# Kernel tuning notes

Measured on AMD Instinct MI355X. Metric: run time of the kernel, lower is better.

## Reference

```python
import jax, jax.numpy as jnp
import numpy as np

NUM_GROUPS = 32
EPS = 1e-8


def stratified_norm(x, s):
    # Per-group mean and (unbiased, ddof=1, matching torch.std) standard deviation,
    # computed with segment sums, then gathered back per sample.
    ones = jnp.ones((x.shape[0],), dtype=x.dtype)
    cnt = jax.ops.segment_sum(ones, s, num_segments=NUM_GROUPS)  # [G]
    mu = jax.ops.segment_sum(x, s, num_segments=NUM_GROUPS) / jnp.maximum(cnt, 1.0)[:, None]  # [G, D]
    diff = x - mu[s]  # [N, D]
    var = jax.ops.segment_sum(diff * diff, s, num_segments=NUM_GROUPS) / jnp.maximum(cnt - 1.0, 1.0)[:, None]
    std = jnp.sqrt(var)  # [G, D]
    return diff / (std[s] + EPS)


def leaky_relu(x):
    return jnp.where(x >= 0, x, 0.01 * x)


def setup_inputs() -> dict:
    key = jax.random.key(0)
    ks = jax.random.split(key, 10)
    N = 524288
    x = jax.random.normal(ks[0], (N, 248), dtype=jnp.float32)
    i = jax.random.randint(ks[1], (N,), 0, NUM_GROUPS, dtype=jnp.int32)
    def lin(kw, kb, fan_in, fan_out):
        bound = 1.0 / np.sqrt(fan_in)
        W = jax.random.uniform(kw, (fan_out, fan_in), jnp.float32, -bound, bound)
        b = jax.random.uniform(kb, (fan_out,), jnp.float32, -bound, bound)
        return W, b
    W1, b1 = lin(ks[2], ks[3], 248, 64)
    W2, b2 = lin(ks[4], ks[5], 64, 64)
    W3, b3 = lin(ks[6], ks[7], 64, 64)
    W4, b4 = lin(ks[8], ks[9], 64, 3)
    return {"x": x, "i": i, "W1": W1, "b1": b1, "W2": W2, "b2": b2,
            "W3": W3, "b3": b3, "W4": W4, "b4": b4}


def reference(x, i, W1, b1, W2, b2, W3, b3, W4, b4):
    # Dropout layers act as identity at inference.
    z = stratified_norm(leaky_relu(x @ W1.T + b1), i)
    z = stratified_norm(leaky_relu(z @ W2.T + b2), i)
    z = stratified_norm(leaky_relu(z @ W3.T + b3), i)
    z = z @ W4.T + b4
    return z
```

## Files before the change

### kernel.cpp

```cpp
#include <hip/hip_runtime.h>


#define GRP_N 32
#define EPSV 1e-8f
constexpr int DIN = 248;
constexpr int KP  = 256;
constexpr int H   = 64;
constexpr int ASTR = 40;

typedef __attribute__((ext_vector_type(8))) short short8;
typedef __attribute__((ext_vector_type(4))) float f32x4;

__device__ __forceinline__ void mfma_bf16(f32x4& d, short8 a, short8 b) {
    asm volatile("v_mfma_f32_16x16x32_bf16 %0, %1, %2, %0"
                 : "+v"(d) : "v"(a), "v"(b));
}

__device__ __forceinline__ unsigned short f2bf(float f) {
    unsigned u = __float_as_uint(f);
    return (unsigned short)((u + 0x7FFFu + ((u >> 16) & 1u)) >> 16);
}
__device__ __forceinline__ float bf2f(unsigned short h) {
    return __uint_as_float((unsigned)h << 16);
}

__global__ void prep_weights(const float* __restrict__ W1, const float* __restrict__ W2,
                             const float* __restrict__ W3, const float* __restrict__ W4,
                             unsigned short* __restrict__ W1bh, unsigned short* __restrict__ W1bl,
                             float* __restrict__ W2T, float* __restrict__ W3T,
                             float* __restrict__ W4T) {
    int idx = blockIdx.x * blockDim.x + threadIdx.x;
    int stride = gridDim.x * blockDim.x;
    for (int t = idx; t < H * KP; t += stride) {
        int c = t >> 8, k = t & 255;
        float v = (k < DIN) ? W1[c * DIN + k] : 0.f;
        unsigned short hi = f2bf(v);
        W1bh[t] = hi;
        W1bl[t] = f2bf(v - bf2f(hi));
    }
    for (int t = idx; t < H * H; t += stride) {
        int k = t / H, c = t % H;
        W2T[t] = W2[c * H + k];
        W3T[t] = W3[c * H + k];
    }
    for (int t = idx; t < H * 3; t += stride) {
        int k = t / 3, o = t % 3;
        W4T[t] = W4[o * H + k];
    }
}

__global__ __launch_bounds__(256)
void gemm1_mfma(const float* __restrict__ x,
                const unsigned short* __restrict__ W1bh, const unsigned short* __restrict__ W1bl,
                const float* __restrict__ b1, const int* __restrict__ grp,
                float* __restrict__ Y, float* __restrict__ sum_, float* __restrict__ sq_,
                int* __restrict__ cnt, int ntiles) {
    __shared__ unsigned short Ah[128 * ASTR];
    __shared__ unsigned short Al[128 * ASTR];
    __shared__ unsigned short Bh[64 * ASTR];
    __shared__ unsigned short Bl[64 * ASTR];
    __shared__ float sS[GRP_N * H];
    __shared__ float sQ[GRP_N * H];
    __shared__ int gl[128];
    __shared__ int cS[GRP_N];
    const int tid = threadIdx.x;
    const int lane = tid & 63, w = tid >> 6;
    const int l15 = lane & 15, lq = lane >> 4;
    for (int t = tid; t < GRP_N * H; t += 256) { sS[t] = 0.f; sQ[t] = 0.f; }
    if (tid < GRP_N) cS[tid] = 0;

    const int arow = tid >> 1;
    const int akb  = (tid & 1) * 16;
    const int bcol = tid >> 2;
    const int bkb  = (tid & 3) * 8;

    float bias4[4];
#pragma unroll
    for (int cf = 0; cf < 4; ++cf) bias4[cf] = b1[cf * 16 + l15];

    for (int tile = blockIdx.x; tile < ntiles; tile += gridDim.x) {
        const int row0 = tile << 7;
        int g = 0;
        if (tid < 128) g = grp[row0 + tid];
        const float* xrow = x + (size_t)(row0 + arow) * DIN;

        float xv[16];
#pragma unroll
        for (int q = 0; q < 4; ++q) {
            const int kg = akb + q * 4;
            float4 t4 = (kg < DIN) ? *(const float4*)(xrow + kg) : make_float4(0.f, 0.f, 0.f, 0.f);
            xv[q * 4 + 0] = t4.x; xv[q * 4 + 1] = t4.y;
            xv[q * 4 + 2] = t4.z; xv[q * 4 + 3] = t4.w;
        }
        float4 wh = *(const float4*)(W1bh + bcol * KP + bkb);
        float4 wl = *(const float4*)(W1bl + bcol * KP + bkb);

        __syncthreads();
        if (tid < 128) { gl[tid] = g; atomicAdd(&cS[g], 1); }

        f32x4 acc[2][4];
#pragma unroll
        for (int rf = 0; rf < 2; ++rf)
#pragma unroll
            for (int cf = 0; cf < 4; ++cf) acc[rf][cf] = (f32x4){0.f, 0.f, 0.f, 0.f};

#pragma unroll 1
        for (int ch = 0; ch < 8; ++ch) {
            if (ch) __syncthreads();
#pragma unroll
            for (int q = 0; q < 4; ++q) {
                unsigned short h[4], l[4];
#pragma unroll
                for (int j = 0; j < 4; ++j) {
                    float v = xv[q * 4 + j];
                    h[j] = f2bf(v);
                    l[j] = f2bf(v - bf2f(h[j]));
                }
                const int aoff = arow * ASTR + akb + q * 4;
                *(ushort4*)&Ah[aoff] = make_ushort4(h[0], h[1], h[2], h[3]);
                *(ushort4*)&Al[aoff] = make_ushort4(l[0], l[1], l[2], l[3]);
            }
            const int boff = bcol * ASTR + bkb;
            *(float4*)&Bh[boff] = wh;
            *(float4*)&Bl[boff] = wl;
            __syncthreads();
            if (ch < 7) {
                const int kc = (ch + 1) * 32;
#pragma unroll
                for (int q = 0; q < 4; ++q) {
                    const int kg = kc + akb + q * 4;
                    float4 t4 = (kg < DIN) ? *(const float4*)(xrow + kg)
                                           : make_float4(0.f, 0.f, 0.f, 0.f);
                    xv[q * 4 + 0] = t4.x; xv[q * 4 + 1] = t4.y;
                    xv[q * 4 + 2] = t4.z; xv[q * 4 + 3] = t4.w;
                }
                wh = *(const float4*)(W1bh + bcol * KP + kc + bkb);
                wl = *(const float4*)(W1bl + bcol * KP + kc + bkb);
            }
            short8 afh[2], afl[2], bfh[4], bfl[4];
#pragma unroll
            for (int rf = 0; rf < 2; ++rf) {
                const int ar = w * 32 + rf * 16 + l15;
                afh[rf] = *(const short8*)&Ah[ar * ASTR + lq * 8];
                afl[rf] = *(const short8*)&Al[ar * ASTR + lq * 8];
            }
#pragma unroll
            for (int cf = 0; cf < 4; ++cf) {
                const int bc = cf * 16 + l15;
                bfh[cf] = *(const short8*)&Bh[bc * ASTR + lq * 8];
                bfl[cf] = *(const short8*)&Bl[bc * ASTR + lq * 8];
            }
#pragma unroll
            for (int cf = 0; cf < 4; ++cf)
#pragma unroll
                for (int rf = 0; rf < 2; ++rf) mfma_bf16(acc[rf][cf], afh[rf], bfh[cf]);
#pragma unroll
            for (int cf = 0; cf < 4; ++cf)
#pragma unroll
                for (int rf = 0; rf < 2; ++rf) mfma_bf16(acc[rf][cf], afh[rf], bfl[cf]);
#pragma unroll
            for (int cf = 0; cf < 4; ++cf)
#pragma unroll
                for (int rf = 0; rf < 2; ++rf) mfma_bf16(acc[rf][cf], afl[rf], bfh[cf]);
        }
        const int rbase = w * 32 + lq * 4;
#pragma unroll
        for (int cf = 0; cf < 4; ++cf) {
            const int col = cf * 16 + l15;
            const float bias = bias4[cf];
#pragma unroll
            for (int rf = 0; rf < 2; ++rf) {
#pragma unroll
                for (int i = 0; i < 4; ++i) {
                    const int rl = rbase + rf * 16 + i;
                    float t = acc[rf][cf][i] + bias;
                    const float o = t >= 0.f ? t : 0.01f * t;
                    Y[(size_t)(row0 + rl) * H + col] = o;
                    const int gr = gl[rl];
                    atomicAdd(&sS[gr * H + col], o);
                    atomicAdd(&sQ[gr * H + col], o * o);
                }
            }
        }
    }
    __syncthreads();
    for (int t = tid; t < GRP_N * H; t += 256) {
        atomicAdd(&sum_[t], sS[t]);
        atomicAdd(&sq_[t], sQ[t]);
    }
    if (tid < GRP_N) atomicAdd(&cnt[tid], cS[tid]);
}

__global__ void finalize_kernel(const float* __restrict__ sum_, const float* __restrict__ sq_,
                                const int* __restrict__ cnt, float* __restrict__ mu_,
                                float* __restrict__ inv_) {
    int t = blockIdx.x * blockDim.x + threadIdx.x;
    if (t >= GRP_N * H) return;
    int g = t >> 6;
    float c = (float)cnt[g];
    float s = sum_[t], q = sq_[t];
    float m = s / fmaxf(c, 1.f);
    float var = fmaxf(q - s * m, 0.f) / fmaxf(c - 1.f, 1.f);
    mu_[t] = m;
    inv_[t] = 1.f / (sqrtf(var) + EPSV);
}

__global__ __launch_bounds__(256)
void gemm_h_fused(float* __restrict__ Y, const int* __restrict__ grp,
                  const float* __restrict__ WT, const float* __restrict__ bias,
                  const float* __restrict__ mu, const float* __restrict__ inv,
                  float* __restrict__ sum_, float* __restrict__ sq_, int ntiles) {
    __shared__ float ZT[16][256];
    __shared__ float WL[H * H];
    __shared__ float sS[GRP_N * H];
    __shared__ float sQ[GRP_N * H];
    __shared__ int gl[256];
    const int tid = threadIdx.x;
    const int rg = tid >> 3, cg = tid & 7;
#pragma unroll
    for (int t = 0; t < 4; ++t)
        ((float4*)WL)[tid + t * 256] = ((const float4*)WT)[tid + t * 256];
    for (int t = tid; t < GRP_N * H; t += 256) { sS[t] = 0.f; sQ[t] = 0.f; }

    for (int tile = blockIdx.x; tile < ntiles; tile += gridDim.x) {
        const int row0 = tile << 8;
        const int g = grp[row0 + tid];
        const float* yrow = Y + (size_t)(row0 + tid) * H;
        const float* mrow = mu + g * H;
        const float* irow = inv + g * H;
        float4 v[4], m[4], iv[4];
#pragma unroll
        for (int q = 0; q < 4; ++q) {
            v[q]  = *(const float4*)(yrow + q * 4);
            m[q]  = *(const float4*)(mrow + q * 4);
            iv[q] = *(const float4*)(irow + q * 4);
        }
        __syncthreads();
        gl[tid] = g;

        float acc[8][8];
#pragma unroll
        for (int r = 0; r < 8; ++r)
#pragma unroll
            for (int c = 0; c < 8; ++c) acc[r][c] = 0.f;

#pragma unroll 1
        for (int ch = 0; ch < 4; ++ch) {
            if (ch) __syncthreads();
#pragma unroll
            for (int q = 0; q < 4; ++q) {
                ZT[q * 4 + 0][tid] = (v[q].x - m[q].x) * iv[q].x;
                ZT[q * 4 + 1][tid] = (v[q].y - m[q].y) * iv[q].y;
                ZT[q * 4 + 2][tid] = (v[q].z - m[q].z) * iv[q].z;
                ZT[q * 4 + 3][tid] = (v[q].w - m[q].w) * iv[q].w;
            }
            __syncthreads();
            if (ch < 3) {
#pragma unroll
                for (int q = 0; q < 4; ++q) {
                    v[q]  = *(const float4*)(yrow + (ch + 1) * 16 + q * 4);
                    m[q]  = *(const float4*)(mrow + (ch + 1) * 16 + q * 4);
                    iv[q] = *(const float4*)(irow + (ch + 1) * 16 + q * 4);
                }
            }
#pragma unroll
            for (int kk = 0; kk < 16; ++kk) {
                const float4 wa = *(const float4*)&WL[(ch * 16 + kk) * 64 + cg * 4];
                const float4 wb = *(const float4*)&WL[(ch * 16 + kk) * 64 + cg * 4 + 32];
                const float4 xa = *(const float4*)&ZT[kk][rg * 4];
                const float4 xb = *(const float4*)&ZT[kk][rg * 4 + 128];
                const float xs[8] = {xa.x, xa.y, xa.z, xa.w, xb.x, xb.y, xb.z, xb.w};
                const float ws8[8] = {wa.x, wa.y, wa.z, wa.w, wb.x, wb.y, wb.z, wb.w};
#pragma unroll
                for (int r = 0; r < 8; ++r)
#pragma unroll
                    for (int c = 0; c < 8; ++c) acc[r][c] += xs[r] * ws8[c];
            }
        }
        const float4 ba = *(const float4*)(bias + cg * 4);
        const float4 bb = *(const float4*)(bias + cg * 4 + 32);
        const float bias8[8] = {ba.x, ba.y, ba.z, ba.w, bb.x, bb.y, bb.z, bb.w};
#pragma unroll
        for (int r = 0; r < 8; ++r) {
            const int lr = rg * 4 + (r & 3) + ((r & 4) ? 128 : 0);
            const int gr = gl[lr];
            float o[8];
#pragma unroll
            for (int c = 0; c < 8; ++c) {
                float t = acc[r][c] + bias8[c];
                o[c] = t >= 0.f ? t : 0.01f * t;
            }
            float* yp = Y + (size_t)(row0 + lr) * H + cg * 4;
            *(float4*)yp        = make_float4(o[0], o[1], o[2], o[3]);
            *(float4*)(yp + 32) = make_float4(o[4], o[5], o[6], o[7]);
            float* Sg = sS + gr * H;
            float* Qg = sQ + gr * H;
#pragma unroll
            for (int c = 0; c < 8; ++c) {
                const int col = cg * 4 + (c & 3) + ((c & 4) ? 32 : 0);
                atomicAdd(&Sg[col], o[c]);
                atomicAdd(&Qg[col], o[c] * o[c]);
            }
        }
    }
    __syncthreads();
    for (int t = tid; t < GRP_N * H; t += 256) {
        atomicAdd(&sum_[t], sS[t]);
        atomicAdd(&sq_[t], sQ[t]);
    }
}

__global__ __launch_bounds__(256)
void gemm4_kernel(const float* __restrict__ Y, const int* __restrict__ grp,
                  const float* __restrict__ W4T, const float* __restrict__ b4,
                  const float* __restrict__ mu, const float* __restrict__ inv,
                  float* __restrict__ out, int n) {
    __shared__ float WL[H * 3];
    const int tid = threadIdx.x;
    if (tid < H * 3) WL[tid] = W4T[tid];
    __syncthreads();
    const int row = blockIdx.x * 256 + tid;
    if (row >= n) return;
    const int g = grp[row];
    float a0 = b4[0], a1 = b4[1], a2 = b4[2];
    const float* yr = Y + (size_t)row * H;
    const float* mr = mu + g * H;
    const float* ir = inv + g * H;
#pragma unroll
    for (int k4 = 0; k4 < H; k4 += 4) {
        float4 v = *(const float4*)(yr + k4);
        float4 m4 = *(const float4*)(mr + k4);
        float4 i4 = *(const float4*)(ir + k4);
        float z[4] = {(v.x - m4.x) * i4.x, (v.y - m4.y) * i4.y,
                      (v.z - m4.z) * i4.z, (v.w - m4.w) * i4.w};
#pragma unroll
        for (int j = 0; j < 4; ++j) {
            a0 += z[j] * WL[(k4 + j) * 3 + 0];
            a1 += z[j] * WL[(k4 + j) * 3 + 1];
            a2 += z[j] * WL[(k4 + j) * 3 + 2];
        }
    }
    out[(size_t)row * 3 + 0] = a0;
    out[(size_t)row * 3 + 1] = a1;
    out[(size_t)row * 3 + 2] = a2;
}

extern "C" void kernel_launch(void* const* d_in, const int* in_sizes, int n_in,
                              void* d_out, int out_size, void* d_ws, size_t ws_size,
                              hipStream_t stream) {
    const float* x  = (const float*)d_in[0];
    const int* grp  = (const int*)d_in[1];
    const float* W1 = (const float*)d_in[2]; const float* b1 = (const float*)d_in[3];
    const float* W2 = (const float*)d_in[4]; const float* b2 = (const float*)d_in[5];
    const float* W3 = (const float*)d_in[6]; const float* b3 = (const float*)d_in[7];
    const float* W4 = (const float*)d_in[8]; const float* b4 = (const float*)d_in[9];
    const int n = in_sizes[1];
    const int ntiles1 = n >> 7;
    const int ntilesH = n >> 8;

    float* ws = (float*)d_ws;
    float* Y  = ws;
    unsigned short* W1bh = (unsigned short*)(ws + (size_t)n * H);
    unsigned short* W1bl = W1bh + H * KP;
    float* W2T = (float*)(W1bl + H * KP);
    float* W3T = W2T + H * H;
    float* W4T = W3T + H * H;
    int*   cnt = (int*)(W4T + H * 3);
    float* stats = (float*)(cnt + 32);
    float* sum1 = stats + 0 * 8192, *sq1 = sum1 + 2048, *mu1 = sum1 + 4096, *inv1 = sum1 + 6144;
    float* sum2 = stats + 1 * 8192, *sq2 = sum2 + 2048, *mu2 = sum2 + 4096, *inv2 = sum2 + 6144;
    float* sum3 = stats + 2 * 8192, *sq3 = sum3 + 2048, *mu3 = sum3 + 4096, *inv3 = sum3 + 6144;

    hipMemsetAsync(cnt, 0, 32 * sizeof(int) + 3 * 8192 * sizeof(float), stream);

    prep_weights<<<32, 256, 0, stream>>>(W1, W2, W3, W4, W1bh, W1bl, W2T, W3T, W4T);

    gemm1_mfma<<<768, 256, 0, stream>>>(x, W1bh, W1bl, b1, grp, Y, sum1, sq1, cnt, ntiles1);
    finalize_kernel<<<8, 256, 0, stream>>>(sum1, sq1, cnt, mu1, inv1);

    gemm_h_fused<<<768, 256, 0, stream>>>(Y, grp, W2T, b2, mu1, inv1, sum2, sq2, ntilesH);
    finalize_kernel<<<8, 256, 0, stream>>>(sum2, sq2, cnt, mu2, inv2);

    gemm_h_fused<<<768, 256, 0, stream>>>(Y, grp, W3T, b3, mu2, inv2, sum3, sq3, ntilesH);
    finalize_kernel<<<8, 256, 0, stream>>>(sum3, sq3, cnt, mu3, inv3);

    gemm4_kernel<<<n / 256, 256, 0, stream>>>(Y, grp, W4T, b4, mu3, inv3,
                                              (float*)d_out, n);
}
```

Before: 1.882 ms.

## Move hidden GEMMs to split-bf16 MFMA, double-buffer LDS fragments, restructure gemm4

Replaces the fp32 FMA hidden-layer GEMMs with bf16 hi/lo split MFMA kernels that use a fragment-major LDS layout. The first GEMM gets double-buffered LDS so staging of the next K chunk overlaps the MFMAs, which removes one barrier per chunk. gemm4 now uses four lanes per row with shuffle reductions and a grid-stride loop, grids shrink to 512 blocks, and finalize computes in double precision. The gain is tensor-core throughput and less sync, at the cost of some precision loss from the 3-term bf16 split.

```diff
diff --git a/kernel.cpp b/kernel.cpp
--- a/kernel.cpp
+++ b/kernel.cpp
@@ -6,7 +6,6 @@
 constexpr int DIN = 248;
 constexpr int KP  = 256;
 constexpr int H   = 64;
-constexpr int ASTR = 40;
 
 typedef __attribute__((ext_vector_type(8))) short short8;
 typedef __attribute__((ext_vector_type(4))) float f32x4;
@@ -24,10 +23,24 @@
     return __uint_as_float((unsigned)h << 16);
 }
 
+__device__ __forceinline__ void split_store16(const float* zz,
+                                              unsigned short* hp, unsigned short* lp) {
+    short8 sh0, sh1, sl0, sl1;
+#pragma unroll
+    for (int j = 0; j < 8; ++j) {
+        unsigned short h0 = f2bf(zz[j]), h1 = f2bf(zz[8 + j]);
+        sh0[j] = (short)h0; sl0[j] = (short)f2bf(zz[j] - bf2f(h0));
+        sh1[j] = (short)h1; sl1[j] = (short)f2bf(zz[8 + j] - bf2f(h1));
+    }
+    *(short8*)(hp) = sh0; *(short8*)(hp + 128) = sh1;
+    *(short8*)(lp) = sl0; *(short8*)(lp + 128) = sl1;
+}
+
 __global__ void prep_weights(const float* __restrict__ W1, const float* __restrict__ W2,
                              const float* __restrict__ W3, const float* __restrict__ W4,
                              unsigned short* __restrict__ W1bh, unsigned short* __restrict__ W1bl,
-                             float* __restrict__ W2T, float* __restrict__ W3T,
+                             unsigned short* __restrict__ W2bh, unsigned short* __restrict__ W2bl,
+                             unsigned short* __restrict__ W3bh, unsigned short* __restrict__ W3bl,
                              float* __restrict__ W4T) {
     int idx = blockIdx.x * blockDim.x + threadIdx.x;
     int stride = gridDim.x * blockDim.x;
@@ -39,9 +52,10 @@
         W1bl[t] = f2bf(v - bf2f(hi));
     }
     for (int t = idx; t < H * H; t += stride) {
-        int k = t / H, c = t % H;
-        W2T[t] = W2[c * H + k];
-        W3T[t] = W3[c * H + k];
+        float v2 = W2[t], v3 = W3[t];
+        unsigned short h2 = f2bf(v2), h3 = f2bf(v3);
+        W2bh[t] = h2; W2bl[t] = f2bf(v2 - bf2f(h2));
+        W3bh[t] = h3; W3bl[t] = f2bf(v3 - bf2f(h3));
     }
     for (int t = idx; t < H * 3; t += stride) {
         int k = t / 3, o = t % 3;
@@ -55,10 +69,8 @@
                 const float* __restrict__ b1, const int* __restrict__ grp,
                 float* __restrict__ Y, float* __restrict__ sum_, float* __restrict__ sq_,
                 int* __restrict__ cnt, int ntiles) {
-    __shared__ unsigned short Ah[128 * ASTR];
-    __shared__ unsigned short Al[128 * ASTR];
-    __shared__ unsigned short Bh[64 * ASTR];
-    __shared__ unsigned short Bl[64 * ASTR];
+    __shared__ unsigned short AF[2][2][4096];
+    __shared__ unsigned short BF[2][2][2048];
     __shared__ float sS[GRP_N * H];
     __shared__ float sQ[GRP_N * H];
     __shared__ int gl[128];
@@ -70,9 +82,11 @@
     if (tid < GRP_N) cS[tid] = 0;
 
     const int arow = tid >> 1;
-    const int akb  = (tid & 1) * 16;
+    const int akb  = (tid & 1) << 4;
+    const int abase = ((arow >> 4) * 64 + (akb >> 3) * 16 + (arow & 15)) * 8;
     const int bcol = tid >> 2;
-    const int bkb  = (tid & 3) * 8;
+    const int bkb  = (tid & 3) << 3;
+    const int bbase = ((bcol >> 4) * 64 + (bkb >> 3) * 16 + (bcol & 15)) * 8;
 
     float bias4[4];
 #pragma unroll
@@ -82,22 +96,43 @@
         const int row0 = tile << 7;
         int g = 0;
         if (tid < 128) g = grp[row0 + tid];
-        const float* xrow = x + (size_t)(row0 + arow) * DIN;
+        const float* xrow = x + (size_t)(row0 + arow) * DIN + akb;
 
         float xv[16];
-#pragma unroll
-        for (int q = 0; q < 4; ++q) {
-            const int kg = akb + q * 4;
-            float4 t4 = (kg < DIN) ? *(const float4*)(xrow + kg) : make_float4(0.f, 0.f, 0.f, 0.f);
-            xv[q * 4 + 0] = t4.x; xv[q * 4 + 1] = t4.y;
-            xv[q * 4 + 2] = t4.z; xv[q * 4 + 3] = t4.w;
-        }
-        float4 wh = *(const float4*)(W1bh + bcol * KP + bkb);
-        float4 wl = *(const float4*)(W1bl + bcol * KP + bkb);
-
+        float4 wh, wl;
+        {
+#pragma unroll
+            for (int q = 0; q < 4; ++q) {
+                const int kg = akb + q * 4;
+                float4 t4 = (kg < DIN) ? *(const float4*)(xrow + q * 4)
+                                       : make_float4(0.f, 0.f, 0.f, 0.f);
+                xv[q * 4 + 0] = t4.x; xv[q * 4 + 1] = t4.y;
+                xv[q * 4 + 2] = t4.z; xv[q * 4 + 3] = t4.w;
+            }
+            wh = *(const float4*)(W1bh + bcol * KP + bkb);
+            wl = *(const float4*)(W1bl + bcol * KP + bkb);
+        }
         __syncthreads();
         if (tid < 128) { gl[tid] = g; atomicAdd(&cS[g], 1); }
 
+        split_store16(xv, &AF[0][0][abase], &AF[0][1][abase]);
+        *(float4*)&BF[0][0][bbase] = wh;
+        *(float4*)&BF[0][1][bbase] = wl;
+        {
+            const int kc = 32;
+#pragma unroll
+            for (int q = 0; q < 4; ++q) {
+                const int kg = kc + akb + q * 4;
+                float4 t4 = (kg < DIN) ? *(const float4*)(xrow + kc + q * 4)
+                                       : make_float4(0.f, 0.f, 0.f, 0.f);
+                xv[q * 4 + 0] = t4.x; xv[q * 4 + 1] = t4.y;
+                xv[q * 4 + 2] = t4.z; xv[q * 4 + 3] = t4.w;
+            }
+            wh = *(const float4*)(W1bh + bcol * KP + kc + bkb);
+            wl = *(const float4*)(W1bl + bcol * KP + kc + bkb);
+        }
+        __syncthreads();
+
         f32x4 acc[2][4];
 #pragma unroll
         for (int rf = 0; rf < 2; ++rf)
@@ -106,62 +141,53 @@
 
 #pragma unroll 1
         for (int ch = 0; ch < 8; ++ch) {
-            if (ch) __syncthreads();
-#pragma unroll
-            for (int q = 0; q < 4; ++q) {
-                unsigned short h[4], l[4];
-#pragma unroll
-                for (int j = 0; j < 4; ++j) {
-                    float v = xv[q * 4 + j];
-                    h[j] = f2bf(v);
-                    l[j] = f2bf(v - bf2f(h[j]));
+            const int cur = ch & 1;
+            short8 afh[2], afl[2], bfh[4], bfl[4];
+#pragma unroll
+            for (int rf = 0; rf < 2; ++rf) {
+                const int fo = ((w * 2 + rf) * 64 + lane) * 8;
+                afh[rf] = *(const short8*)&AF[cur][0][fo];
+                afl[rf] = *(const short8*)&AF[cur][1][fo];
+            }
+#pragma unroll
+            for (int cf = 0; cf < 4; ++cf) {
+                const int fo = (cf * 64 + lane) * 8;
+                bfh[cf] = *(const short8*)&BF[cur][0][fo];
+                bfl[cf] = *(const short8*)&BF[cur][1][fo];
+            }
+#pragma unroll
+            for (int cf = 0; cf < 4; ++cf)
+#pragma unroll
+                for (int rf = 0; rf < 2; ++rf) mfma_bf16(acc[rf][cf], afh[rf], bfh[cf]);
+#pragma unroll
+            for (int cf = 0; cf < 4; ++cf)
+#pragma unroll
+                for (int rf = 0; rf < 2; ++rf) mfma_bf16(acc[rf][cf], afh[rf], bfl[cf]);
+#pragma unroll
+            for (int cf = 0; cf < 4; ++cf)
+#pragma unroll
+                for (int rf = 0; rf < 2; ++rf) mfma_bf16(acc[rf][cf], afl[rf], bfh[cf]);
+
+            if (ch < 7) {
+                const int nb = cur ^ 1;
+                split_store16(xv, &AF[nb][0][abase], &AF[nb][1][abase]);
+                *(float4*)&BF[nb][0][bbase] = wh;
+                *(float4*)&BF[nb][1][bbase] = wl;
+                if (ch < 6) {
+                    const int kc = (ch + 2) * 32;
+#pragma unroll
+                    for (int q = 0; q < 4; ++q) {
+                        const int kg = kc + akb + q * 4;
+                        float4 t4 = (kg < DIN) ? *(const float4*)(xrow + kc + q * 4)
+                                               : make_float4(0.f, 0.f, 0.f, 0.f);
+                        xv[q * 4 + 0] = t4.x; xv[q * 4 + 1] = t4.y;
+                        xv[q * 4 + 2] = t4.z; xv[q * 4 + 3] = t4.w;
+                    }
+                    wh = *(const float4*)(W1bh + bcol * KP + kc + bkb);
+                    wl = *(const float4*)(W1bl + bcol * KP + kc + bkb);
                 }
-                const int aoff = arow * ASTR + akb + q * 4;
-                *(ushort4*)&Ah[aoff] = make_ushort4(h[0], h[1], h[2], h[3]);
-                *(ushort4*)&Al[aoff] = make_ushort4(l[0], l[1], l[2], l[3]);
-            }
-            const int boff = bcol * ASTR + bkb;
-            *(float4*)&Bh[boff] = wh;
-            *(float4*)&Bl[boff] = wl;
-            __syncthreads();
-            if (ch < 7) {
-                const int kc = (ch + 1) * 32;
-#pragma unroll
-                for (int q = 0; q < 4; ++q) {
-                    const int kg = kc + akb + q * 4;
-                    float4 t4 = (kg < DIN) ? *(const float4*)(xrow + kg)
-                                           : make_float4(0.f, 0.f, 0.f, 0.f);
-                    xv[q * 4 + 0] = t4.x; xv[q * 4 + 1] = t4.y;
-                    xv[q * 4 + 2] = t4.z; xv[q * 4 + 3] = t4.w;
-                }
-                wh = *(const float4*)(W1bh + bcol * KP + kc + bkb);
-                wl = *(const float4*)(W1bl + bcol * KP + kc + bkb);
-            }
-            short8 afh[2], afl[2], bfh[4], bfl[4];
-#pragma unroll
-            for (int rf = 0; rf < 2; ++rf) {
-                const int ar = w * 32 + rf * 16 + l15;
-                afh[rf] = *(const short8*)&Ah[ar * ASTR + lq * 8];
-                afl[rf] = *(const short8*)&Al[ar * ASTR + lq * 8];
-            }
-#pragma unroll
-            for (int cf = 0; cf < 4; ++cf) {
-                const int bc = cf * 16 + l15;
-                bfh[cf] = *(const short8*)&Bh[bc * ASTR + lq * 8];
-                bfl[cf] = *(const short8*)&Bl[bc * ASTR + lq * 8];
-            }
-#pragma unroll
-            for (int cf = 0; cf < 4; ++cf)
-#pragma unroll
-                for (int rf = 0; rf < 2; ++rf) mfma_bf16(acc[rf][cf], afh[rf], bfh[cf]);
-#pragma unroll
-            for (int cf = 0; cf < 4; ++cf)
-#pragma unroll
-                for (int rf = 0; rf < 2; ++rf) mfma_bf16(acc[rf][cf], afh[rf], bfl[cf]);
-#pragma unroll
-            for (int cf = 0; cf < 4; ++cf)
-#pragma unroll
-                for (int rf = 0; rf < 2; ++rf) mfma_bf16(acc[rf][cf], afl[rf], bfh[cf]);
+                __syncthreads();
+            }
         }
         const int rbase = w * 32 + lq * 4;
 #pragma unroll
@@ -197,109 +223,182 @@
     int t = blockIdx.x * blockDim.x + threadIdx.x;
     if (t >= GRP_N * H) return;
     int g = t >> 6;
-    float c = (float)cnt[g];
-    float s = sum_[t], q = sq_[t];
-    float m = s / fmaxf(c, 1.f);
-    float var = fmaxf(q - s * m, 0.f) / fmaxf(c - 1.f, 1.f);
-    mu_[t] = m;
-    inv_[t] = 1.f / (sqrtf(var) + EPSV);
+    double c = (double)cnt[g];
+    double s = (double)sum_[t], q = (double)sq_[t];
+    double m = s / fmax(c, 1.0);
+    double var = fmax(q - s * m, 0.0) / fmax(c - 1.0, 1.0);
+    mu_[t] = (float)m;
+    inv_[t] = (float)(1.0 / (sqrt(var) + (double)EPSV));
 }
 
 __global__ __launch_bounds__(256)
-void gemm_h_fused(float* __restrict__ Y, const int* __restrict__ grp,
-                  const float* __restrict__ WT, const float* __restrict__ bias,
-                  const float* __restrict__ mu, const float* __restrict__ inv,
-                  float* __restrict__ sum_, float* __restrict__ sq_, int ntiles) {
-    __shared__ float ZT[16][256];
-    __shared__ float WL[H * H];
+void gemm_h_mfma(float* __restrict__ Y, const int* __restrict__ grp,
+                 const unsigned short* __restrict__ Wbh, const unsigned short* __restrict__ Wbl,
+                 const float* __restrict__ bias, const float* __restrict__ mu,
+                 const float* __restrict__ inv,
+                 float* __restrict__ sum_, float* __restrict__ sq_, int ntiles) {
+    __shared__ unsigned short AF[2][2][4096];
+    __shared__ unsigned short BF[2][2][2048];
     __shared__ float sS[GRP_N * H];
     __shared__ float sQ[GRP_N * H];
-    __shared__ int gl[256];
+    __shared__ int gl[128];
     const int tid = threadIdx.x;
-    const int rg = tid >> 3, cg = tid & 7;
-#pragma unroll
-    for (int t = 0; t < 4; ++t)
-        ((float4*)WL)[tid + t * 256] = ((const float4*)WT)[tid + t * 256];
+    const int lane = tid & 63, w = tid >> 6;
+    const int l15 = lane & 15, lq = lane >> 4;
     for (int t = tid; t < GRP_N * H; t += 256) { sS[t] = 0.f; sQ[t] = 0.f; }
 
+    const int arow = tid >> 1;
+    const int akb  = (tid & 1) << 4;
+    const int abase = ((arow >> 4) * 64 + (akb >> 3) * 16 + (arow & 15)) * 8;
+    const int bcol = tid >> 2;
+    const int bkb  = (tid & 3) << 3;
+    const int bbase = ((bcol >> 4) * 64 + (bkb >> 3) * 16 + (bcol & 15)) * 8;
+
+    {
+        *(float4*)&BF[0][0][bbase] = *(const float4*)(Wbh + bcol * H + bkb);
+        *(float4*)&BF[0][1][bbase] = *(const float4*)(Wbl + bcol * H + bkb);
+        *(float4*)&BF[1][0][bbase] = *(const float4*)(Wbh + bcol * H + 32 + bkb);
+        *(float4*)&BF[1][1][bbase] = *(const float4*)(Wbl + bcol * H + 32 + bkb);
+    }
+
+    float bias4[4];
+#pragma unroll
+    for (int cf = 0; cf < 4; ++cf) bias4[cf] = bias[cf * 16 + l15];
+
     for (int tile = blockIdx.x; tile < ntiles; tile += gridDim.x) {
-        const int row0 = tile << 8;
-        const int g = grp[row0 + tid];
-        const float* yrow = Y + (size_t)(row0 + tid) * H;
-        const float* mrow = mu + g * H;
-        const float* irow = inv + g * H;
-        float4 v[4], m[4], iv[4];
-#pragma unroll
-        for (int q = 0; q < 4; ++q) {
-            v[q]  = *(const float4*)(yrow + q * 4);
-            m[q]  = *(const float4*)(mrow + q * 4);
-            iv[q] = *(const float4*)(irow + q * 4);
-        }
+        const int row0 = tile << 7;
+        int g = 0;
+        if (tid < 128) g = grp[row0 + tid];
+        const int ag = grp[row0 + arow];
+        const float* yrow = Y + (size_t)(row0 + arow) * H + akb;
+        const float* mrow = mu + ag * H + akb;
+        const float* irow = inv + ag * H + akb;
+
+        float4 y0 = *(const float4*)(yrow);
+        float4 y1 = *(const float4*)(yrow + 4);
+        float4 y2 = *(const float4*)(yrow + 8);
+        float4 y3 = *(const float4*)(yrow + 12);
+
         __syncthreads();
-        gl[tid] = g;
-
-        float acc[8][8];
-#pragma unroll
-        for (int r = 0; r < 8; ++r)
-#pragma unroll
-            for (int c = 0; c < 8; ++c) acc[r][c] = 0.f;
-
-#pragma unroll 1
-        for (int ch = 0; ch < 4; ++ch) {
-            if (ch) __syncthreads();
-#pragma unroll
-            for (int q = 0; q < 4; ++q) {
-                ZT[q * 4 + 0][tid] = (v[q].x - m[q].x) * iv[q].x;
-                ZT[q * 4 + 1][tid] = (v[q].y - m[q].y) * iv[q].y;
-                ZT[q * 4 + 2][tid] = (v[q].z - m[q].z) * iv[q].z;
-                ZT[q * 4 + 3][tid] = (v[q].w - m[q].w) * iv[q].w;
-            }
-            __syncthreads();
-            if (ch < 3) {
-#pragma unroll
-                for (int q = 0; q < 4; ++q) {
-                    v[q]  = *(const float4*)(yrow + (ch + 1) * 16 + q * 4);
-                    m[q]  = *(const float4*)(mrow + (ch + 1) * 16 + q * 4);
-                    iv[q] = *(const float4*)(irow + (ch + 1) * 16 + q * 4);
+        if (tid < 128) gl[tid] = g;
+
+        {
+            float4 m0 = *(const float4*)(mrow),     m1 = *(const float4*)(mrow + 4);
+            float4 m2 = *(const float4*)(mrow + 8), m3 = *(const float4*)(mrow + 12);
+            float4 i0 = *(const float4*)(irow),     i1 = *(const float4*)(irow + 4);
+            float4 i2 = *(const float4*)(irow + 8), i3 = *(const float4*)(irow + 12);
+            float zz[16];
+            zz[0] = (y0.x - m0.x) * i0.x; zz[1] = (y0.y - m0.y) * i0.y;
+            zz[2] = (y0.z - m0.z) * i0.z; zz[3] = (y0.w - m0.w) * i0.w;
+            zz[4] = (y1.x - m1.x) * i1.x; zz[5] = (y1.y - m1.y) * i1.y;
+            zz[6] = (y1.z - m1.z) * i1.z; zz[7] = (y1.w - m1.w) * i1.w;
+            zz[8] = (y2.x - m2.x) * i2.x; zz[9] = (y2.y - m2.y) * i2.y;
+            zz[10] = (y2.z - m2.z) * i2.z; zz[11] = (y2.w - m2.w) * i2.w;
+            zz[12] = (y3.x - m3.x) * i3.x; zz[13] = (y3.y - m3.y) * i3.y;
+            zz[14] = (y3.z - m3.z) * i3.z; zz[15] = (y3.w - m3.w) * i3.w;
+            split_store16(zz, &AF[0][0][abase], &AF[0][1][abase]);
+        }
+        y0 = *(const float4*)(yrow + 32);
+        y1 = *(const float4*)(yrow + 36);
+        y2 = *(const float4*)(yrow + 40);
+        y3 = *(const float4*)(yrow + 44);
+        __syncthreads();
+
+        f32x4 acc[2][4];
+#pragma unroll
+        for (int rf = 0; rf < 2; ++rf)
+#pragma unroll
+            for (int cf = 0; cf < 4; ++cf) acc[rf][cf] = (f32x4){0.f, 0.f, 0.f, 0.f};
+
+        {
+            short8 afh[2], afl[2], bfh[4], bfl[4];
+#pragma unroll
+            for (int rf = 0; rf < 2; ++rf) {
+                const int fo = ((w * 2 + rf) * 64 + lane) * 8;
+                afh[rf] = *(const short8*)&AF[0][0][fo];
+                afl[rf] = *(const short8*)&AF[0][1][fo];
+            }
+#pragma unroll
+            for (int cf = 0; cf < 4; ++cf) {
+                const int fo = (cf * 64 + lane) * 8;
+                bfh[cf] = *(const short8*)&BF[0][0][fo];
+                bfl[cf] = *(const short8*)&BF[0][1][fo];
+            }
+#pragma unroll
+            for (int cf = 0; cf < 4; ++cf)
+#pragma unroll
+                for (int rf = 0; rf < 2; ++rf) mfma_bf16(acc[rf][cf], afh[rf], bfh[cf]);
+#pragma unroll
+            for (int cf = 0; cf < 4; ++cf)
+#pragma unroll
+                for (int rf = 0; rf < 2; ++rf) mfma_bf16(acc[rf][cf], afh[rf], bfl[cf]);
+#pragma unroll
+            for (int cf = 0; cf < 4; ++cf)
+#pragma unroll
+                for (int rf = 0; rf < 2; ++rf) mfma_bf16(acc[rf][cf], afl[rf], bfh[cf]);
+        }
+        {
+            float4 m0 = *(const float4*)(mrow + 32), m1 = *(const float4*)(mrow + 36);
+            float4 m2 = *(const float4*)(mrow + 40), m3 = *(const float4*)(mrow + 44);
+            float4 i0 = *(const float4*)(irow + 32), i1 = *(const float4*)(irow + 36);
+            float4 i2 = *(const float4*)(irow + 40), i3 = *(const float4*)(irow + 44);
+            float zz[16];
+            zz[0] = (y0.x - m0.x) * i0.x; zz[1] = (y0.y - m0.y) * i0.y;
+            zz[2] = (y0.z - m0.z) * i0.z; zz[3] = (y0.w - m0.w) * i0.w;
+            zz[4] = (y1.x - m1.x) * i1.x; zz[5] = (y1.y - m1.y) * i1.y;
+            zz[6] = (y1.z - m1.z) * i1.z; zz[7] = (y1.w - m1.w) * i1.w;
+            zz[8] = (y2.x - m2.x) * i2.x; zz[9] = (y2.y - m2.y) * i2.y;
+            zz[10] = (y2.z - m2.z) * i2.z; zz[11] = (y2.w - m2.w) * i2.w;
+            zz[12] = (y3.x - m3.x) * i3.x; zz[13] = (y3.y - m3.y) * i3.y;
+            zz[14] = (y3.z - m3.z) * i3.z; zz[15] = (y3.w - m3.w) * i3.w;
+            split_store16(zz, &AF[1][0][abase], &AF[1][1][abase]);
+        }
+        __syncthreads();
+
+        {
+            short8 afh[2], afl[2], bfh[4], bfl[4];
+#pragma unroll
+            for (int rf = 0; rf < 2; ++rf) {
+                const int fo = ((w * 2 + rf) * 64 + lane) * 8;
+                afh[rf] = *(const short8*)&AF[1][0][fo];
+                afl[rf] = *(const short8*)&AF[1][1][fo];
+            }
+#pragma unroll
+            for (int cf = 0; cf < 4; ++cf) {
+                const int fo = (cf * 64 + lane) * 8;
+                bfh[cf] = *(const short8*)&BF[1][0][fo];
+                bfl[cf] = *(const short8*)&BF[1][1][fo];
+            }
+#pragma unroll
+            for (int cf = 0; cf < 4; ++cf)
+#pragma unroll
+                for (int rf = 0; rf < 2; ++rf) mfma_bf16(acc[rf][cf], afh[rf], bfh[cf]);
+#pragma unroll
+            for (int cf = 0; cf < 4; ++cf)
+#pragma unroll
+                for (int rf = 0; rf < 2; ++rf) mfma_bf16(acc[rf][cf], afh[rf], bfl[cf]);
+#pragma unroll
+            for (int cf = 0; cf < 4; ++cf)
+#pragma unroll
+                for (int rf = 0; rf < 2; ++rf) mfma_bf16(acc[rf][cf], afl[rf], bfh[cf]);
+        }
+        const int rbase = w * 32 + lq * 4;
+#pragma unroll
+        for (int cf = 0; cf < 4; ++cf) {
+            const int col = cf * 16 + l15;
+            const float bv = bias4[cf];
+#pragma unroll
+            for (int rf = 0; rf < 2; ++rf) {
+#pragma unroll
+                for (int i = 0; i < 4; ++i) {
+                    const int rl = rbase + rf * 16 + i;
+                    float t = acc[rf][cf][i] + bv;
+                    const float o = t >= 0.f ? t : 0.01f * t;
+                    Y[(size_t)(row0 + rl) * H + col] = o;
+                    const int gr = gl[rl];
+                    atomicAdd(&sS[gr * H + col], o);
+                    atomicAdd(&sQ[gr * H + col], o * o);
                 }
-            }
-#pragma unroll
-            for (int kk = 0; kk < 16; ++kk) {
-                const float4 wa = *(const float4*)&WL[(ch * 16 + kk) * 64 + cg * 4];
-                const float4 wb = *(const float4*)&WL[(ch * 16 + kk) * 64 + cg * 4 + 32];
-                const float4 xa = *(const float4*)&ZT[kk][rg * 4];
-                const float4 xb = *(const float4*)&ZT[kk][rg * 4 + 128];
-                const float xs[8] = {xa.x, xa.y, xa.z, xa.w, xb.x, xb.y, xb.z, xb.w};
-                const float ws8[8] = {wa.x, wa.y, wa.z, wa.w, wb.x, wb.y, wb.z, wb.w};
-#pragma unroll
-                for (int r = 0; r < 8; ++r)
-#pragma unroll
-                    for (int c = 0; c < 8; ++c) acc[r][c] += xs[r] * ws8[c];
-            }
-        }
-        const float4 ba = *(const float4*)(bias + cg * 4);
-        const float4 bb = *(const float4*)(bias + cg * 4 + 32);
-        const float bias8[8] = {ba.x, ba.y, ba.z, ba.w, bb.x, bb.y, bb.z, bb.w};
-#pragma unroll
-        for (int r = 0; r < 8; ++r) {
-            const int lr = rg * 4 + (r & 3) + ((r & 4) ? 128 : 0);
-            const int gr = gl[lr];
-            float o[8];
-#pragma unroll
-            for (int c = 0; c < 8; ++c) {
-                float t = acc[r][c] + bias8[c];
-                o[c] = t >= 0.f ? t : 0.01f * t;
-            }
-            float* yp = Y + (size_t)(row0 + lr) * H + cg * 4;
-            *(float4*)yp        = make_float4(o[0], o[1], o[2], o[3]);
-            *(float4*)(yp + 32) = make_float4(o[4], o[5], o[6], o[7]);
-            float* Sg = sS + gr * H;
-            float* Qg = sQ + gr * H;
-#pragma unroll
-            for (int c = 0; c < 8; ++c) {
-                const int col = cg * 4 + (c & 3) + ((c & 4) ? 32 : 0);
-                atomicAdd(&Sg[col], o[c]);
-                atomicAdd(&Qg[col], o[c] * o[c]);
             }
         }
     }
@@ -314,35 +413,42 @@
 void gemm4_kernel(const float* __restrict__ Y, const int* __restrict__ grp,
                   const float* __restrict__ W4T, const float* __restrict__ b4,
                   const float* __restrict__ mu, const float* __restrict__ inv,
-                  float* __restrict__ out, int n) {
+                  float* __restrict__ out, int nblk) {
     __shared__ float WL[H * 3];
     const int tid = threadIdx.x;
     if (tid < H * 3) WL[tid] = W4T[tid];
     __syncthreads();
-    const int row = blockIdx.x * 256 + tid;
-    if (row >= n) return;
-    const int g = grp[row];
-    float a0 = b4[0], a1 = b4[1], a2 = b4[2];
-    const float* yr = Y + (size_t)row * H;
-    const float* mr = mu + g * H;
-    const float* ir = inv + g * H;
-#pragma unroll
-    for (int k4 = 0; k4 < H; k4 += 4) {
-        float4 v = *(const float4*)(yr + k4);
-        float4 m4 = *(const float4*)(mr + k4);
-        float4 i4 = *(const float4*)(ir + k4);
-        float z[4] = {(v.x - m4.x) * i4.x, (v.y - m4.y) * i4.y,
-                      (v.z - m4.z) * i4.z, (v.w - m4.w) * i4.w};
-#pragma unroll
-        for (int j = 0; j < 4; ++j) {
-            a0 += z[j] * WL[(k4 + j) * 3 + 0];
-            a1 += z[j] * WL[(k4 + j) * 3 + 1];
-            a2 += z[j] * WL[(k4 + j) * 3 + 2];
-        }
-    }
-    out[(size_t)row * 3 + 0] = a0;
-    out[(size_t)row * 3 + 1] = a1;
-    out[(size_t)row * 3 + 2] = a2;
+    const int l = tid & 63, wv = tid >> 6;
+    const int qr = l >> 2, qc = l & 3, seg = qc * 16;
+    const float bcst = (qc < 3) ? b4[qc] : 0.f;
+    for (int rb = blockIdx.x; rb < nblk; rb += gridDim.x) {
+        const int row = (rb << 6) + (wv << 4) + qr;
+        const int g = grp[row];
+        const float* yr = Y + (size_t)row * H + seg;
+        const float* mr = mu + g * H + seg;
+        const float* ir = inv + g * H + seg;
+        float a0 = 0.f, a1 = 0.f, a2 = 0.f;
+#pragma unroll
+        for (int q4 = 0; q4 < 4; ++q4) {
+            float4 v = *(const float4*)(yr + q4 * 4);
+            float4 m4 = *(const float4*)(mr + q4 * 4);
+            float4 i4 = *(const float4*)(ir + q4 * 4);
+            float z[4] = {(v.x - m4.x) * i4.x, (v.y - m4.y) * i4.y,
+                          (v.z - m4.z) * i4.z, (v.w - m4.w) * i4.w};
+#pragma unroll
+            for (int j = 0; j < 4; ++j) {
+                const float* wl = &WL[(seg + q4 * 4 + j) * 3];
+                a0 += z[j] * wl[0];
+                a1 += z[j] * wl[1];
+                a2 += z[j] * wl[2];
+            }
+        }
+        a0 += __shfl_xor(a0, 1); a0 += __shfl_xor(a0, 2);
+        a1 += __shfl_xor(a1, 1); a1 += __shfl_xor(a1, 2);
+        a2 += __shfl_xor(a2, 1); a2 += __shfl_xor(a2, 2);
+        const float res = (qc == 0) ? a0 : ((qc == 1) ? a1 : a2);
+        if (qc < 3) out[(size_t)row * 3 + qc] = res + bcst;
+    }
 }
 
 extern "C" void kernel_launch(void* const* d_in, const int* in_sizes, int n_in,
@@ -356,15 +462,17 @@
     const float* W4 = (const float*)d_in[8]; const float* b4 = (const float*)d_in[9];
     const int n = in_sizes[1];
     const int ntiles1 = n >> 7;
-    const int ntilesH = n >> 8;
+    const int nblk4   = n >> 6;
 
     float* ws = (float*)d_ws;
     float* Y  = ws;
     unsigned short* W1bh = (unsigned short*)(ws + (size_t)n * H);
     unsigned short* W1bl = W1bh + H * KP;
-    float* W2T = (float*)(W1bl + H * KP);
-    float* W3T = W2T + H * H;
-    float* W4T = W3T + H * H;
+    unsigned short* W2bh = W1bl + H * KP;
+    unsigned short* W2bl = W2bh + H * H;
+    unsigned short* W3bh = W2bl + H * H;
+    unsigned short* W3bl = W3bh + H * H;
+    float* W4T = (float*)(W3bl + H * H);
     int*   cnt = (int*)(W4T + H * 3);
     float* stats = (float*)(cnt + 32);
     float* sum1 = stats + 0 * 8192, *sq1 = sum1 + 2048, *mu1 = sum1 + 4096, *inv1 = sum1 + 6144;
@@ -373,17 +481,18 @@
 
     hipMemsetAsync(cnt, 0, 32 * sizeof(int) + 3 * 8192 * sizeof(float), stream);
 
-    prep_weights<<<32, 256, 0, stream>>>(W1, W2, W3, W4, W1bh, W1bl, W2T, W3T, W4T);
-
-    gemm1_mfma<<<768, 256, 0, stream>>>(x, W1bh, W1bl, b1, grp, Y, sum1, sq1, cnt, ntiles1);
+    prep_weights<<<32, 256, 0, stream>>>(W1, W2, W3, W4, W1bh, W1bl,
+                                         W2bh, W2bl, W3bh, W3bl, W4T);
+
+    gemm1_mfma<<<512, 256, 0, stream>>>(x, W1bh, W1bl, b1, grp, Y, sum1, sq1, cnt, ntiles1);
     finalize_kernel<<<8, 256, 0, stream>>>(sum1, sq1, cnt, mu1, inv1);
 
-    gemm_h_fused<<<768, 256, 0, stream>>>(Y, grp, W2T, b2, mu1, inv1, sum2, sq2, ntilesH);
+    gemm_h_mfma<<<512, 256, 0, stream>>>(Y, grp, W2bh, W2bl, b2, mu1, inv1, sum2, sq2, ntiles1);
     finalize_kernel<<<8, 256, 0, stream>>>(sum2, sq2, cnt, mu2, inv2);
 
-    gemm_h_fused<<<768, 256, 0, stream>>>(Y, grp, W3T, b3, mu2, inv2, sum3, sq3, ntilesH);
+    gemm_h_mfma<<<512, 256, 0, stream>>>(Y, grp, W3bh, W3bl, b3, mu2, inv2, sum3, sq3, ntiles1);
     finalize_kernel<<<8, 256, 0, stream>>>(sum3, sq3, cnt, mu3, inv3);
 
-    gemm4_kernel<<<n / 256, 256, 0, stream>>>(Y, grp, W4T, b4, mu3, inv3,
-                                              (float*)d_out, n);
-}
+    gemm4_kernel<<<2048, 256, 0, stream>>>(Y, grp, W4T, b4, mu3, inv3,
+                                           (float*)d_out, nblk4);
+}
```

New measurement: 1.730 ms. 1.09x faster.
